# Performance work log

Hardware: AMD Instinct MI355X
Metric: run time of the kernel (lower is better)

Reference implementation:

```python
import jax, jax.numpy as jnp
import numpy as np

B, C2D, C3D, H, W, N = 4, 64, 64, 256, 256, 16384
NEG_SLOPE = 0.1


def _conv1x1_lrelu(x, w, b):
    # 1x1 conv (no norm) + leaky_relu(0.1), per Conv2dNormRelu defaults
    y = jnp.einsum('bchw,oc->bohw', x, w) + b[None, :, None, None]
    return jax.nn.leaky_relu(y, NEG_SLOPE)


def _batch_gather(feat, idx):
    # feat: [B, C, N], idx: [B, P] -> [B, C, P]
    return jnp.take_along_axis(feat, idx[:, None, :], axis=2)


def setup_inputs() -> dict:
    key = jax.random.key(0)
    ks = jax.random.split(key, 14)
    f = jax.random.normal
    s = 0.05
    return {
        'xy': jax.random.uniform(ks[0], (B, 2, N), jnp.float32) * jnp.float32(W),
        'feat_2d': f(ks[1], (B, C2D, H, W), jnp.float32),
        'feat_3d': f(ks[2], (B, C3D, N), jnp.float32),
        'last_flow_2d': f(ks[3], (B, 2, H, W), jnp.float32),
        'last_flow_3d_to_2d': f(ks[4], (B, 2, N), jnp.float32),
        'nn_proj': jax.random.randint(ks[5], (B, H, W, 1), 0, N, jnp.int32),
        'w1': f(ks[6], (C3D, C3D + 5), jnp.float32) * s,
        'b1': f(ks[7], (C3D,), jnp.float32) * s,
        'w2': f(ks[8], (C3D, C3D), jnp.float32) * s,
        'b2': f(ks[9], (C3D,), jnp.float32) * s,
        'w3': f(ks[10], (C3D, C3D), jnp.float32) * s,
        'b3': f(ks[11], (C3D,), jnp.float32) * s,
        'wf': f(ks[12], (C2D, C2D + C3D), jnp.float32) * s,
        'bf': f(ks[13], (C2D,), jnp.float32) * s,
    }


def reference(xy, feat_2d, feat_3d, last_flow_2d, last_flow_3d_to_2d, nn_proj,
              w1, b1, w2, b2, w3, b3, wf, bf):
    b, _, h, w = feat_2d.shape
    # concat per-point flow onto 3D features: [B, C3D+2, N]
    feat_3d_aug = jnp.concatenate([feat_3d, last_flow_3d_to_2d], axis=1)

    idx = nn_proj[..., 0].reshape(b, h * w)  # nearest-neighbor point per pixel
    gathered = _batch_gather(feat_3d_aug, idx).reshape(b, -1, h, w)  # [B, C3D+2, H, W]
    xy_proj = _batch_gather(xy, idx).reshape(b, 2, h, w)             # [B, 2, H, W]

    # pixel-coordinate mesh grid: channel 0 = x (width), channel 1 = y (height)
    gy, gx = jnp.meshgrid(jnp.arange(h, dtype=xy.dtype), jnp.arange(w, dtype=xy.dtype), indexing='ij')
    grid = jnp.stack([gx, gy], axis=0)[None]  # [1, 2, H, W]
    offset = xy_proj - grid                    # [B, 2, H, W]

    # correlation between gathered 3D feats and 2D feats (channel mean)
    corr = jnp.mean(gathered[:, :C2D] * feat_2d, axis=1, keepdims=True)  # [B, 1, H, W]

    # last 2 channels are the projected flow; subtract detached last_flow_2d
    flow_ch = gathered[:, -2:] - jax.lax.stop_gradient(last_flow_2d)
    x = jnp.concatenate([corr, offset, gathered[:, :-2], flow_ch], axis=1)  # [B, C3D+5, H, W]

    x = _conv1x1_lrelu(x, w1, b1)
    x = _conv1x1_lrelu(x, w2, b2)
    x = _conv1x1_lrelu(x, w3, b3)
    out = _conv1x1_lrelu(jnp.concatenate([x, feat_2d], axis=1), wf, bf)  # [B, C2D, H, W]
    return out
```

## Files before the change

kernel.cpp:

```cpp
#include <hip/hip_runtime.h>

#define BB 4
#define CH 64
#define HW 65536
#define NN 16384
#define NT 128
#define XPITCH 104
#define W1OFS 0
#define W2OFS 6144
#define W3OFS 10240
#define WFOFS 14336
#define FWS_BYTE 46080
#define PTAB_BYTE 49152
#define PT_ROW 160
#define WS_NEED ((size_t)PTAB_BYTE + (size_t)BB * NN * PT_ROW)

typedef __attribute__((ext_vector_type(8))) short short8;
typedef __attribute__((ext_vector_type(4))) float f32x4;

union frag_u { unsigned short u[8]; short8 v; };
union row_u  { uint4 q[4]; unsigned short u[32]; };

static __device__ __forceinline__ unsigned short f2bf(float x) {
    unsigned int u = __float_as_uint(x);
    return (unsigned short)((u + 0x7fffu + ((u >> 16) & 1u)) >> 16);
}
static __device__ __forceinline__ float bf2f(unsigned short h) {
    return __uint_as_float(((unsigned int)h) << 16);
}

__global__ __launch_bounds__(256) void prep_w(
    const float* __restrict__ w1, const float* __restrict__ b1,
    const float* __restrict__ w2, const float* __restrict__ b2,
    const float* __restrict__ w3, const float* __restrict__ b3,
    const float* __restrict__ wf, const float* __restrict__ bf,
    unsigned short* __restrict__ wpk, float* __restrict__ fws)
{
    const int t = threadIdx.x;
    for (int i = t; i < 64 * 96; i += 256) {
        const int m = i / 96, k = i % 96;
        float v = 0.f;
        if (k < 64) v = w1[m * 69 + 3 + k];
        else if (k == 64) v = w1[m * 69 + 0];
        else if (k == 67) v = w1[m * 69 + 67];
        else if (k == 68) v = w1[m * 69 + 68];
        wpk[W1OFS + i] = f2bf(v);
    }
    for (int i = t; i < 64 * 64; i += 256) wpk[W2OFS + i] = f2bf(w2[i]);
    for (int i = t; i < 64 * 64; i += 256) wpk[W3OFS + i] = f2bf(w3[i]);
    for (int i = t; i < 64 * 128; i += 256) wpk[WFOFS + i] = f2bf(wf[i]);
    if (t < 64) {
        fws[t]       = b1[t];
        fws[64 + t]  = b2[t];
        fws[128 + t] = b3[t];
        fws[192 + t] = bf[t];
        fws[256 + t] = w1[t * 69 + 1];
        fws[320 + t] = w1[t * 69 + 2];
    }
}

__global__ __launch_bounds__(256) void prep_t(
    const float* __restrict__ xy, const float* __restrict__ f3d,
    const float* __restrict__ lf3d, char* __restrict__ pt)
{
    const int gn = blockIdx.x * 256 + threadIdx.x;
    const int b = blockIdx.y;
    row_u r0, r1;
#pragma unroll
    for (int c = 0; c < 32; c++) r0.u[c] = f2bf(f3d[(size_t)(b * CH + c) * NN + gn]);
#pragma unroll
    for (int c = 0; c < 32; c++) r1.u[c] = f2bf(f3d[(size_t)(b * CH + 32 + c) * NN + gn]);
    char* row = pt + ((size_t)b * NN + gn) * PT_ROW;
    uint4* rq = (uint4*)row;
#pragma unroll
    for (int k = 0; k < 4; k++) rq[k] = r0.q[k];
#pragma unroll
    for (int k = 0; k < 4; k++) rq[4 + k] = r1.q[k];
    float4 e;
    e.x = xy[(size_t)(b * 2 + 0) * NN + gn];
    e.y = xy[(size_t)(b * 2 + 1) * NN + gn];
    e.z = lf3d[(size_t)(b * 2 + 0) * NN + gn];
    e.w = lf3d[(size_t)(b * 2 + 1) * NN + gn];
    *(float4*)(row + 144) = e;
}

template<int KT, int KROW, bool LO>
static __device__ __forceinline__ void layer_mfma(
    const unsigned short* __restrict__ wrow,
    const unsigned short* Xh, const unsigned short* Xl,
    int w, int ln, int q, f32x4 acc[4][2])
{
#pragma unroll
    for (int kt = 0; kt < KT; kt++) {
        const int kcol = kt * 32 + q * 8;
        short8 A[4];
#pragma unroll
        for (int mi = 0; mi < 4; mi++)
            A[mi] = *(const short8*)(wrow + (mi * 16 + ln) * KROW + kcol);
#pragma unroll
        for (int ni = 0; ni < 2; ni++) {
            const int nr = 32 * w + ni * 16 + ln;
            short8 bh = *(const short8*)(Xh + nr * XPITCH + kcol);
            short8 bl = bh;
            if (LO) bl = *(const short8*)(Xl + nr * XPITCH + kcol);
#pragma unroll
            for (int mi = 0; mi < 4; mi++) {
                acc[mi][ni] = __builtin_amdgcn_mfma_f32_16x16x32_bf16(A[mi], bh, acc[mi][ni], 0, 0, 0);
                if (LO)
                    acc[mi][ni] = __builtin_amdgcn_mfma_f32_16x16x32_bf16(A[mi], bl, acc[mi][ni], 0, 0, 0);
            }
        }
    }
}

static __device__ __forceinline__ void zero_acc(f32x4 acc[4][2]) {
#pragma unroll
    for (int mi = 0; mi < 4; mi++)
#pragma unroll
        for (int ni = 0; ni < 2; ni++)
#pragma unroll
            for (int r = 0; r < 4; r++) acc[mi][ni][r] = 0.f;
}

static __device__ __forceinline__ void epi_x(
    f32x4 acc[4][2], const float* __restrict__ fws, int bofs, bool off_fix,
    const float* offsp, unsigned short* Xh, unsigned short* Xl,
    int w, int ln, int q)
{
#pragma unroll
    for (int mi = 0; mi < 4; mi++) {
        const float4 bias = *(const float4*)(fws + bofs + mi * 16 + q * 4);
        float4 wox = bias, woy = bias;
        if (off_fix) {
            wox = *(const float4*)(fws + 256 + mi * 16 + q * 4);
            woy = *(const float4*)(fws + 320 + mi * 16 + q * 4);
        }
#pragma unroll
        for (int ni = 0; ni < 2; ni++) {
            const int nr = 32 * w + ni * 16 + ln;
            float ox = 0.f, oy = 0.f;
            if (off_fix) { ox = offsp[nr]; oy = offsp[NT + nr]; }
            unsigned int hh0 = 0, hh1 = 0, ll0 = 0, ll1 = 0;
#pragma unroll
            for (int r = 0; r < 4; r++) {
                float a = acc[mi][ni][r] + ((const float*)&bias)[r];
                if (off_fix) a += ((const float*)&wox)[r] * ox + ((const float*)&woy)[r] * oy;
                a = fmaxf(a, 0.1f * a);
                const unsigned short hb = f2bf(a);
                const unsigned short lb = f2bf(a - bf2f(hb));
                if (r == 0) { hh0 = hb; ll0 = lb; }
                if (r == 1) { hh0 |= ((unsigned)hb) << 16; ll0 |= ((unsigned)lb) << 16; }
                if (r == 2) { hh1 = hb; ll1 = lb; }
                if (r == 3) { hh1 |= ((unsigned)hb) << 16; ll1 |= ((unsigned)lb) << 16; }
            }
            *(uint2*)&Xh[nr * XPITCH + mi * 16 + q * 4] = make_uint2(hh0, hh1);
            *(uint2*)&Xl[nr * XPITCH + mi * 16 + q * 4] = make_uint2(ll0, ll1);
        }
    }
}

__global__ __launch_bounds__(256, 2) void fuse(
    const float* __restrict__ feat2d, const float* __restrict__ lf2d,
    const int* __restrict__ nn,
    const unsigned short* __restrict__ wpk, const float* __restrict__ fws,
    const char* __restrict__ ptab,
    float* __restrict__ out)
{
    __shared__ unsigned short Xhi[NT * XPITCH];
    __shared__ unsigned short Xlo[NT * XPITCH];
    __shared__ float corrP[2 * NT];
    __shared__ float offsS[2 * NT];
    __shared__ float fcfS[2 * NT];
    __shared__ int idxL[NT];

    const int tid = threadIdx.x;
    const int w = tid >> 6, lane = tid & 63;
    const int q = lane >> 4, ln = lane & 15;
    const int b = blockIdx.y;
    const int p0 = blockIdx.x * NT;

    if (w == 0) {
        idxL[lane] = nn[(size_t)b * HW + p0 + lane];
        idxL[64 + lane] = nn[(size_t)b * HW + p0 + 64 + lane];
    }
    __syncthreads();

    {
        const int h = w >> 1, cp = w & 1;
        const int n = h * 64 + lane;
        const int p = p0 + n;
        const int idx = idxL[n];
        const char* prow = ptab + ((size_t)b * NN + idx) * PT_ROW;
        row_u g;
#pragma unroll
        for (int k = 0; k < 4; k++) g.q[k] = ((const uint4*)prow)[cp * 4 + k];
        float ca = 0.f;
#pragma unroll
        for (int i = 0; i < 32; i++) {
            const int c = cp * 32 + i;
            const float f = feat2d[(size_t)(b * CH + c) * HW + p];
            ca += f * bf2f(g.u[i]);
        }
        corrP[cp * NT + n] = ca;
        uint4* xp = (uint4*)&Xhi[n * XPITCH + cp * 32];
#pragma unroll
        for (int k = 0; k < 4; k++) xp[k] = g.q[k];
        if (cp == 0) {
            const float4 e = *(const float4*)(prow + 144);
            offsS[n] = e.x - (float)(p & 255);
            offsS[NT + n] = e.y - (float)(p >> 8);
            fcfS[n] = e.z - lf2d[(size_t)(b * 2 + 0) * HW + p];
            fcfS[NT + n] = e.w - lf2d[(size_t)(b * 2 + 1) * HW + p];
        }
    }
    __syncthreads();
    if ((w & 1) == 0) {
        const int n = (w >> 1) * 64 + lane;
        const float corr = (corrP[n] + corrP[NT + n]) * (1.0f / 64.0f);
        const unsigned short chh = f2bf(corr);
        const unsigned short xhh = f2bf(fcfS[n]);
        const unsigned short yhh = f2bf(fcfS[NT + n]);
        uint4* tp = (uint4*)&Xhi[n * XPITCH + 64];
        tp[0] = make_uint4((unsigned)chh, ((unsigned)xhh) << 16, (unsigned)yhh, 0u);
        tp[1] = make_uint4(0, 0, 0, 0);
        tp[2] = make_uint4(0, 0, 0, 0);
        tp[3] = make_uint4(0, 0, 0, 0);
    }
    __syncthreads();

    f32x4 acc[4][2];
    zero_acc(acc);
    layer_mfma<3, 96, false>(wpk + W1OFS, Xhi, Xlo, w, ln, q, acc);
    epi_x(acc, fws, 0, true, offsS, Xhi, Xlo, w, ln, q);
    zero_acc(acc);
    layer_mfma<2, 64, true>(wpk + W2OFS, Xhi, Xlo, w, ln, q, acc);
    epi_x(acc, fws, 64, false, offsS, Xhi, Xlo, w, ln, q);
    zero_acc(acc);
    layer_mfma<2, 64, true>(wpk + W3OFS, Xhi, Xlo, w, ln, q, acc);
    epi_x(acc, fws, 128, false, offsS, Xhi, Xlo, w, ln, q);
    zero_acc(acc);
    layer_mfma<2, 128, true>(wpk + WFOFS, Xhi, Xlo, w, ln, q, acc);
#pragma unroll
    for (int kt = 2; kt < 4; kt++) {
        const int kcol = kt * 32 + q * 8;
        short8 A[4];
#pragma unroll
        for (int mi = 0; mi < 4; mi++)
            A[mi] = *(const short8*)(wpk + WFOFS + (mi * 16 + ln) * 128 + kcol);
#pragma unroll
        for (int ni = 0; ni < 2; ni++) {
            frag_u fh;
#pragma unroll
            for (int j = 0; j < 8; j++) {
                const int c = (kt - 2) * 32 + q * 8 + j;
                const float v = feat2d[(size_t)(b * CH + c) * HW + p0 + 32 * w + ni * 16 + ln];
                fh.u[j] = f2bf(v);
            }
#pragma unroll
            for (int mi = 0; mi < 4; mi++)
                acc[mi][ni] = __builtin_amdgcn_mfma_f32_16x16x32_bf16(A[mi], fh.v, acc[mi][ni], 0, 0, 0);
        }
    }
#pragma unroll
    for (int mi = 0; mi < 4; mi++) {
        const float4 bias = *(const float4*)(fws + 192 + mi * 16 + q * 4);
#pragma unroll
        for (int ni = 0; ni < 2; ni++) {
#pragma unroll
            for (int r = 0; r < 4; r++) {
                float a = acc[mi][ni][r] + ((const float*)&bias)[r];
                a = fmaxf(a, 0.1f * a);
                const int m = mi * 16 + q * 4 + r;
                out[(size_t)(b * CH + m) * HW + p0 + 32 * w + ni * 16 + ln] = a;
            }
        }
    }
}

__global__ __launch_bounds__(256) void fuse_slow(
    const float* __restrict__ feat2d, const float* __restrict__ lf2d,
    const float* __restrict__ xy, const float* __restrict__ feat3d,
    const float* __restrict__ lf3d, const int* __restrict__ nn,
    const float* __restrict__ w1, const float* __restrict__ b1,
    const float* __restrict__ w2, const float* __restrict__ b2,
    const float* __restrict__ w3, const float* __restrict__ b3,
    const float* __restrict__ wf, const float* __restrict__ bfv,
    float* __restrict__ out)
{
    const int p = blockIdx.x * 256 + threadIdx.x;
    const int b = blockIdx.y;
    const int idx = nn[(size_t)b * HW + p];
    const float* f3 = feat3d + (size_t)b * CH * NN + idx;
    float g[CH];
#pragma unroll
    for (int c = 0; c < CH; c++) g[c] = f3[(size_t)c * NN];
    const float fl3x = lf3d[(size_t)(b * 2 + 0) * NN + idx];
    const float fl3y = lf3d[(size_t)(b * 2 + 1) * NN + idx];
    const float xyx = xy[(size_t)(b * 2 + 0) * NN + idx];
    const float xyy = xy[(size_t)(b * 2 + 1) * NN + idx];
    const float* f2p = feat2d + (size_t)b * CH * HW + p;
    float corr = 0.f;
#pragma unroll
    for (int c = 0; c < CH; c++) corr += f2p[(size_t)c * HW] * g[c];
    corr *= (1.f / 64.f);
    float xin[69];
    xin[0] = corr;
    xin[1] = xyx - (float)(p & 255);
    xin[2] = xyy - (float)(p >> 8);
#pragma unroll
    for (int c = 0; c < CH; c++) xin[3 + c] = g[c];
    xin[67] = fl3x - lf2d[(size_t)(b * 2 + 0) * HW + p];
    xin[68] = fl3y - lf2d[(size_t)(b * 2 + 1) * HW + p];
    float x1[64], x2[64], x3[64], accv[64];
#pragma unroll
    for (int o = 0; o < 64; o++) {
        float a = b1[o];
#pragma unroll
        for (int k = 0; k < 69; k++) a += w1[o * 69 + k] * xin[k];
        x1[o] = (a >= 0.f) ? a : 0.1f * a;
    }
#pragma unroll
    for (int o = 0; o < 64; o++) {
        float a = b2[o];
#pragma unroll
        for (int k = 0; k < 64; k++) a += w2[o * 64 + k] * x1[k];
        x2[o] = (a >= 0.f) ? a : 0.1f * a;
    }
#pragma unroll
    for (int o = 0; o < 64; o++) {
        float a = b3[o];
#pragma unroll
        for (int k = 0; k < 64; k++) a += w3[o * 64 + k] * x2[k];
        x3[o] = (a >= 0.f) ? a : 0.1f * a;
    }
#pragma unroll
    for (int o = 0; o < 64; o++) {
        float a = bfv[o];
#pragma unroll
        for (int k = 0; k < 64; k++) a += wf[o * 128 + k] * x3[k];
        accv[o] = a;
    }
#pragma unroll
    for (int k = 0; k < 64; k++) {
        const float f = f2p[(size_t)k * HW];
#pragma unroll
        for (int o = 0; o < 64; o++) accv[o] += wf[o * 128 + 64 + k] * f;
    }
#pragma unroll
    for (int o = 0; o < 64; o++) {
        float a = accv[o];
        a = (a >= 0.f) ? a : 0.1f * a;
        out[(size_t)(b * CH + o) * HW + p] = a;
    }
}

extern "C" void kernel_launch(void* const* d_in, const int* in_sizes, int n_in,
                              void* d_out, int out_size, void* d_ws, size_t ws_size,
                              hipStream_t stream)
{
    const float* xy   = (const float*)d_in[0];
    const float* f2d  = (const float*)d_in[1];
    const float* f3d  = (const float*)d_in[2];
    const float* lf2d = (const float*)d_in[3];
    const float* lf3d = (const float*)d_in[4];
    const int*   nn   = (const int*)d_in[5];
    const float* w1 = (const float*)d_in[6];
    const float* b1 = (const float*)d_in[7];
    const float* w2 = (const float*)d_in[8];
    const float* b2 = (const float*)d_in[9];
    const float* w3 = (const float*)d_in[10];
    const float* b3 = (const float*)d_in[11];
    const float* wf = (const float*)d_in[12];
    const float* bf = (const float*)d_in[13];

    if (ws_size >= WS_NEED) {
        unsigned short* wpk = (unsigned short*)d_ws;
        float* fws = (float*)((char*)d_ws + FWS_BYTE);
        char* pt = (char*)d_ws + PTAB_BYTE;
        prep_w<<<1, 256, 0, stream>>>(w1, b1, w2, b2, w3, b3, wf, bf, wpk, fws);
        prep_t<<<dim3(NN / 256, BB), 256, 0, stream>>>(xy, f3d, lf3d, pt);
        fuse<<<dim3(HW / NT, BB), 256, 0, stream>>>(f2d, lf2d, nn, wpk, fws, pt, (float*)d_out);
    } else {
        fuse_slow<<<dim3(HW / 256, BB), 256, 0, stream>>>(f2d, lf2d, xy, f3d, lf3d, nn,
                                                          w1, b1, w2, b2, w3, b3, wf, bf,
                                                          (float*)d_out);
    }
}
```

Baseline: 246.6 us.

## Alias layer-one input buffer with hi/lo buffers and merge prep kernels

Shared memory is shrunk by overlaying the wide first-layer input tile (pitch 104) with the hi/lo activation buffers (pitch 72). A barrier is added after layer one so the overlay is safe. Launch bounds go from 2 to 4 blocks per SM to raise occupancy. The weight-packing and point-table prep kernels are merged into one launch with an extra block column, which removes one kernel launch. Asking for more blocks per SM may force register spilling, and the extra barrier adds a synchronisation point.

```diff
diff --git a/kernel.cpp b/kernel.cpp
--- a/kernel.cpp
+++ b/kernel.cpp
@@ -5,7 +5,8 @@
 #define HW 65536
 #define NN 16384
 #define NT 128
-#define XPITCH 104
+#define XP0 104
+#define XP 72
 #define W1OFS 0
 #define W2OFS 6144
 #define W3OFS 10240
@@ -29,41 +30,41 @@
     return __uint_as_float(((unsigned int)h) << 16);
 }
 
-__global__ __launch_bounds__(256) void prep_w(
+__global__ __launch_bounds__(256) void prep(
+    const float* __restrict__ xy, const float* __restrict__ f3d,
+    const float* __restrict__ lf3d,
     const float* __restrict__ w1, const float* __restrict__ b1,
     const float* __restrict__ w2, const float* __restrict__ b2,
     const float* __restrict__ w3, const float* __restrict__ b3,
     const float* __restrict__ wf, const float* __restrict__ bf,
-    unsigned short* __restrict__ wpk, float* __restrict__ fws)
+    char* __restrict__ pt, unsigned short* __restrict__ wpk, float* __restrict__ fws)
 {
     const int t = threadIdx.x;
-    for (int i = t; i < 64 * 96; i += 256) {
-        const int m = i / 96, k = i % 96;
-        float v = 0.f;
-        if (k < 64) v = w1[m * 69 + 3 + k];
-        else if (k == 64) v = w1[m * 69 + 0];
-        else if (k == 67) v = w1[m * 69 + 67];
-        else if (k == 68) v = w1[m * 69 + 68];
-        wpk[W1OFS + i] = f2bf(v);
-    }
-    for (int i = t; i < 64 * 64; i += 256) wpk[W2OFS + i] = f2bf(w2[i]);
-    for (int i = t; i < 64 * 64; i += 256) wpk[W3OFS + i] = f2bf(w3[i]);
-    for (int i = t; i < 64 * 128; i += 256) wpk[WFOFS + i] = f2bf(wf[i]);
-    if (t < 64) {
-        fws[t]       = b1[t];
-        fws[64 + t]  = b2[t];
-        fws[128 + t] = b3[t];
-        fws[192 + t] = bf[t];
-        fws[256 + t] = w1[t * 69 + 1];
-        fws[320 + t] = w1[t * 69 + 2];
-    }
-}
-
-__global__ __launch_bounds__(256) void prep_t(
-    const float* __restrict__ xy, const float* __restrict__ f3d,
-    const float* __restrict__ lf3d, char* __restrict__ pt)
-{
-    const int gn = blockIdx.x * 256 + threadIdx.x;
+    if (blockIdx.x == NN / 256) {
+        if (blockIdx.y != 0) return;
+        for (int i = t; i < 64 * 96; i += 256) {
+            const int m = i / 96, k = i % 96;
+            float v = 0.f;
+            if (k < 64) v = w1[m * 69 + 3 + k];
+            else if (k == 64) v = w1[m * 69 + 0];
+            else if (k == 67) v = w1[m * 69 + 67];
+            else if (k == 68) v = w1[m * 69 + 68];
+            wpk[W1OFS + i] = f2bf(v);
+        }
+        for (int i = t; i < 64 * 64; i += 256) wpk[W2OFS + i] = f2bf(w2[i]);
+        for (int i = t; i < 64 * 64; i += 256) wpk[W3OFS + i] = f2bf(w3[i]);
+        for (int i = t; i < 64 * 128; i += 256) wpk[WFOFS + i] = f2bf(wf[i]);
+        if (t < 64) {
+            fws[t]       = b1[t];
+            fws[64 + t]  = b2[t];
+            fws[128 + t] = b3[t];
+            fws[192 + t] = bf[t];
+            fws[256 + t] = w1[t * 69 + 1];
+            fws[320 + t] = w1[t * 69 + 2];
+        }
+        return;
+    }
+    const int gn = blockIdx.x * 256 + t;
     const int b = blockIdx.y;
     row_u r0, r1;
 #pragma unroll
@@ -84,7 +85,7 @@
     *(float4*)(row + 144) = e;
 }
 
-template<int KT, int KROW, bool LO>
+template<int KT, int KROW, int PITCH, bool LO>
 static __device__ __forceinline__ void layer_mfma(
     const unsigned short* __restrict__ wrow,
     const unsigned short* Xh, const unsigned short* Xl,
@@ -100,9 +101,9 @@
 #pragma unroll
         for (int ni = 0; ni < 2; ni++) {
             const int nr = 32 * w + ni * 16 + ln;
-            short8 bh = *(const short8*)(Xh + nr * XPITCH + kcol);
+            short8 bh = *(const short8*)(Xh + nr * PITCH + kcol);
             short8 bl = bh;
-            if (LO) bl = *(const short8*)(Xl + nr * XPITCH + kcol);
+            if (LO) bl = *(const short8*)(Xl + nr * PITCH + kcol);
 #pragma unroll
             for (int mi = 0; mi < 4; mi++) {
                 acc[mi][ni] = __builtin_amdgcn_mfma_f32_16x16x32_bf16(A[mi], bh, acc[mi][ni], 0, 0, 0);
@@ -153,25 +154,28 @@
                 if (r == 2) { hh1 = hb; ll1 = lb; }
                 if (r == 3) { hh1 |= ((unsigned)hb) << 16; ll1 |= ((unsigned)lb) << 16; }
             }
-            *(uint2*)&Xh[nr * XPITCH + mi * 16 + q * 4] = make_uint2(hh0, hh1);
-            *(uint2*)&Xl[nr * XPITCH + mi * 16 + q * 4] = make_uint2(ll0, ll1);
-        }
-    }
-}
-
-__global__ __launch_bounds__(256, 2) void fuse(
+            *(uint2*)&Xh[nr * XP + mi * 16 + q * 4] = make_uint2(hh0, hh1);
+            *(uint2*)&Xl[nr * XP + mi * 16 + q * 4] = make_uint2(ll0, ll1);
+        }
+    }
+}
+
+__global__ __launch_bounds__(256, 4) void fuse(
     const float* __restrict__ feat2d, const float* __restrict__ lf2d,
     const int* __restrict__ nn,
     const unsigned short* __restrict__ wpk, const float* __restrict__ fws,
     const char* __restrict__ ptab,
     float* __restrict__ out)
 {
-    __shared__ unsigned short Xhi[NT * XPITCH];
-    __shared__ unsigned short Xlo[NT * XPITCH];
+    __shared__ unsigned short Xbuf[2 * NT * XP];
     __shared__ float corrP[2 * NT];
     __shared__ float offsS[2 * NT];
     __shared__ float fcfS[2 * NT];
     __shared__ int idxL[NT];
+
+    unsigned short* X0 = Xbuf;
+    unsigned short* Xh = Xbuf;
+    unsigned short* Xl = Xbuf + NT * XP;
 
     const int tid = threadIdx.x;
     const int w = tid >> 6, lane = tid & 63;
@@ -179,10 +183,7 @@
     const int b = blockIdx.y;
     const int p0 = blockIdx.x * NT;
 
-    if (w == 0) {
-        idxL[lane] = nn[(size_t)b * HW + p0 + lane];
-        idxL[64 + lane] = nn[(size_t)b * HW + p0 + 64 + lane];
-    }
+    if (tid < NT) idxL[tid] = nn[(size_t)b * HW + p0 + tid];
     __syncthreads();
 
     {
@@ -202,7 +203,7 @@
             ca += f * bf2f(g.u[i]);
         }
         corrP[cp * NT + n] = ca;
-        uint4* xp = (uint4*)&Xhi[n * XPITCH + cp * 32];
+        uint4* xp = (uint4*)&X0[n * XP0 + cp * 32];
 #pragma unroll
         for (int k = 0; k < 4; k++) xp[k] = g.q[k];
         if (cp == 0) {
@@ -220,7 +221,7 @@
         const unsigned short chh = f2bf(corr);
         const unsigned short xhh = f2bf(fcfS[n]);
         const unsigned short yhh = f2bf(fcfS[NT + n]);
-        uint4* tp = (uint4*)&Xhi[n * XPITCH + 64];
+        uint4* tp = (uint4*)&X0[n * XP0 + 64];
         tp[0] = make_uint4((unsigned)chh, ((unsigned)xhh) << 16, (unsigned)yhh, 0u);
         tp[1] = make_uint4(0, 0, 0, 0);
         tp[2] = make_uint4(0, 0, 0, 0);
@@ -230,16 +231,17 @@
 
     f32x4 acc[4][2];
     zero_acc(acc);
-    layer_mfma<3, 96, false>(wpk + W1OFS, Xhi, Xlo, w, ln, q, acc);
-    epi_x(acc, fws, 0, true, offsS, Xhi, Xlo, w, ln, q);
+    layer_mfma<3, 96, XP0, false>(wpk + W1OFS, X0, X0, w, ln, q, acc);
+    __syncthreads();
+    epi_x(acc, fws, 0, true, offsS, Xh, Xl, w, ln, q);
     zero_acc(acc);
-    layer_mfma<2, 64, true>(wpk + W2OFS, Xhi, Xlo, w, ln, q, acc);
-    epi_x(acc, fws, 64, false, offsS, Xhi, Xlo, w, ln, q);
+    layer_mfma<2, 64, XP, true>(wpk + W2OFS, Xh, Xl, w, ln, q, acc);
+    epi_x(acc, fws, 64, false, offsS, Xh, Xl, w, ln, q);
     zero_acc(acc);
-    layer_mfma<2, 64, true>(wpk + W3OFS, Xhi, Xlo, w, ln, q, acc);
-    epi_x(acc, fws, 128, false, offsS, Xhi, Xlo, w, ln, q);
+    layer_mfma<2, 64, XP, true>(wpk + W3OFS, Xh, Xl, w, ln, q, acc);
+    epi_x(acc, fws, 128, false, offsS, Xh, Xl, w, ln, q);
     zero_acc(acc);
-    layer_mfma<2, 128, true>(wpk + WFOFS, Xhi, Xlo, w, ln, q, acc);
+    layer_mfma<2, 128, XP, true>(wpk + WFOFS, Xh, Xl, w, ln, q, acc);
 #pragma unroll
     for (int kt = 2; kt < 4; kt++) {
         const int kcol = kt * 32 + q * 8;
@@ -377,8 +379,9 @@
         unsigned short* wpk = (unsigned short*)d_ws;
         float* fws = (float*)((char*)d_ws + FWS_BYTE);
         char* pt = (char*)d_ws + PTAB_BYTE;
-        prep_w<<<1, 256, 0, stream>>>(w1, b1, w2, b2, w3, b3, wf, bf, wpk, fws);
-        prep_t<<<dim3(NN / 256, BB), 256, 0, stream>>>(xy, f3d, lf3d, pt);
+        prep<<<dim3(NN / 256 + 1, BB), 256, 0, stream>>>(xy, f3d, lf3d,
+                                                         w1, b1, w2, b2, w3, b3, wf, bf,
+                                                         pt, wpk, fws);
         fuse<<<dim3(HW / NT, BB), 256, 0, stream>>>(f2d, lf2d, nn, wpk, fws, pt, (float*)d_out);
     } else {
         fuse_slow<<<dim3(HW / 256, BB), 256, 0, stream>>>(f2d, lf2d, xy, f3d, lf3d, nn,
```

New measurement: 247.2 us. Within noise of the previous version (+0.2%).
